# Optimization experiments

Measured on AMD Instinct MI355X. Metric: run time of the kernel, lower is better.

The kernel has to match this reference:

```python
import jax, jax.numpy as jnp
import numpy as np

N0, N1, N2, B = 1500000, 200000, 20000, 4096


def sage_conv(x_src, x_dst, src, dst, Wl, Wr, b, n_dst):
    # mean-aggregate neighbor features onto targets, then two linears + bias
    msg = x_src[src]                                             # [E, d]
    agg = jax.ops.segment_sum(msg, dst, num_segments=n_dst)       # [n_dst, d]
    cnt = jax.ops.segment_sum(jnp.ones(src.shape[0], x_src.dtype), dst, num_segments=n_dst)
    mean = agg / jnp.maximum(cnt, 1.0)[:, None]
    return mean @ Wl + x_dst @ Wr + b


def setup_inputs() -> dict:
    key = jax.random.key(0)
    ks = jax.random.split(key, 16)
    d_in, d_h, d_out = 100, 256, 47
    s = lambda k, sh, fan: jax.random.normal(k, sh, jnp.float32) * (1.0 / np.sqrt(fan))
    return {
        "x": jax.random.normal(ks[0], (N0, d_in), jnp.float32),
        "src0": jax.random.randint(ks[1], (2000000,), 0, N0),
        "dst0": jax.random.randint(ks[2], (2000000,), 0, N1),
        "src1": jax.random.randint(ks[3], (200000,), 0, N1),
        "dst1": jax.random.randint(ks[4], (200000,), 0, N2),
        "src2": jax.random.randint(ks[5], (20480,), 0, N2),
        "dst2": jax.random.randint(ks[6], (20480,), 0, B),
        "Wl0": s(ks[7], (d_in, d_h), d_in),
        "Wr0": s(ks[8], (d_in, d_h), d_in),
        "b0": jnp.zeros((d_h,), jnp.float32),
        "Wl1": s(ks[9], (d_h, d_h), d_h),
        "Wr1": s(ks[10], (d_h, d_h), d_h),
        "b1": jnp.zeros((d_h,), jnp.float32),
        "Wl2": s(ks[11], (d_h, d_out), d_h),
        "Wr2": s(ks[12], (d_h, d_out), d_h),
        "b2": jnp.zeros((d_out,), jnp.float32),
    }


def reference(x, src0, dst0, src1, dst1, src2, dst2,
              Wl0, Wr0, b0, Wl1, Wr1, b1, Wl2, Wr2, b2):
    # layer 0: sources = all sampled nodes, targets = first N1 nodes
    h = sage_conv(x, x[:N1], src0, dst0, Wl0, Wr0, b0, N1)
    h = jax.nn.relu(h)  # dropout is identity in eval mode
    # layer 1
    h = sage_conv(h, h[:N2], src1, dst1, Wl1, Wr1, b1, N2)
    h = jax.nn.relu(h)
    # layer 2 (final)
    h = sage_conv(h, h[:B], src2, dst2, Wl2, Wr2, b2, B)
    return jax.nn.log_softmax(h, axis=-1)
```

## Files before the change

### kernel.cpp

```cpp
#include <hip/hip_runtime.h>
#include <hip/hip_bf16.h>

#define N0   1500000
#define N1   200000
#define N2   20000
#define NB   4096
#define D_IN 100
#define D_H  256
#define D_OUT 47

#define K0P  224
#define K12P 512

#define SCAN_BLOCKS 256

typedef __bf16 bf16x8 __attribute__((ext_vector_type(8)));
typedef __bf16 bf16x4 __attribute__((ext_vector_type(4)));
typedef float  f32x4  __attribute__((ext_vector_type(4)));

__global__ void hist_kernel(const int* __restrict__ dst, int* __restrict__ deg, int E)
{
    int i = blockIdx.x * blockDim.x + threadIdx.x;
    if (i < E) atomicAdd(&deg[dst[i]], 1);
}

__global__ __launch_bounds__(256)
void scan_partial(const int* __restrict__ deg, int* __restrict__ partials, int n)
{
    const int b = blockIdx.x;
    const int chunk = (n + gridDim.x - 1) / gridDim.x;
    const int begin = b * chunk;
    const int end = min(begin + chunk, n);

    int s = 0;
    for (int i = begin + threadIdx.x; i < end; i += blockDim.x) s += deg[i];

    #pragma unroll
    for (int o = 32; o > 0; o >>= 1) s += __shfl_down(s, o);
    __shared__ int wsum[4];
    if ((threadIdx.x & 63) == 0) wsum[threadIdx.x >> 6] = s;
    __syncthreads();
    if (threadIdx.x == 0)
        partials[b] = wsum[0] + wsum[1] + wsum[2] + wsum[3];
}

__global__ __launch_bounds__(256)
void scan_offsets(int* __restrict__ partials, int* __restrict__ rowstart, int n)
{
    __shared__ int sm[256];
    const int t = threadIdx.x;
    sm[t] = partials[t];
    __syncthreads();
    for (int d = 1; d < 256; d <<= 1) {
        int val = sm[t];
        int oth = (t >= d) ? sm[t - d] : 0;
        __syncthreads();
        sm[t] = val + oth;
        __syncthreads();
    }
    partials[t] = (t > 0) ? sm[t - 1] : 0;
    if (t == 0) rowstart[n] = sm[255];
}

__global__ __launch_bounds__(256)
void scan_apply(const int* __restrict__ deg, const int* __restrict__ offsets,
                int* __restrict__ rowstart, int n)
{
    const int b = blockIdx.x;
    const int chunk = (n + gridDim.x - 1) / gridDim.x;
    const int begin = b * chunk;
    const int end = min(begin + chunk, n);

    __shared__ int sm[256];
    const int sub = (chunk + blockDim.x - 1) / blockDim.x;
    const int tb = begin + threadIdx.x * sub;
    const int te = min(tb + sub, end);

    int s = 0;
    for (int i = tb; i < te; ++i) s += deg[i];
    sm[threadIdx.x] = s;
    __syncthreads();
    for (int d = 1; d < 256; d <<= 1) {
        int val = sm[threadIdx.x];
        int oth = (threadIdx.x >= d) ? sm[threadIdx.x - d] : 0;
        __syncthreads();
        sm[threadIdx.x] = val + oth;
        __syncthreads();
    }
    int run = offsets[b] + ((threadIdx.x > 0) ? sm[threadIdx.x - 1] : 0);
    for (int i = tb; i < te; ++i) { rowstart[i] = run; run += deg[i]; }
}

__global__ void scatter_kernel(const int* __restrict__ src,
                               const int* __restrict__ dst,
                               const int* __restrict__ rowstart,
                               int* __restrict__ cursor,
                               int* __restrict__ csr_src, int E)
{
    int i = blockIdx.x * blockDim.x + threadIdx.x;
    if (i < E) {
        int t = dst[i];
        int pos = rowstart[t] + atomicAdd(&cursor[t], 1);
        csr_src[pos] = src[i];
    }
}

__global__ __launch_bounds__(256)
void gather_pack_l0(const float* __restrict__ x,
                    const int* __restrict__ rowstart,
                    const int* __restrict__ csr_src,
                    __bf16* __restrict__ A0, int nrows)
{
    const int wid  = (blockIdx.x * blockDim.x + threadIdx.x) >> 6;
    const int lane = threadIdx.x & 63;
    if (wid >= nrows) return;

    const int beg = rowstart[wid];
    const int end = rowstart[wid + 1];
    const bool act = lane < D_IN / 2;
    const int f = lane * 2;

    float ax[8], ay[8];
    #pragma unroll
    for (int u = 0; u < 8; ++u) { ax[u] = 0.0f; ay[u] = 0.0f; }

    int e = beg;
    for (; e + 8 <= end; e += 8) {
        int idx[8];
        #pragma unroll
        for (int u = 0; u < 8; ++u) idx[u] = csr_src[e + u];
        if (act) {
            float2 p[8];
            #pragma unroll
            for (int u = 0; u < 8; ++u)
                p[u] = *reinterpret_cast<const float2*>(x + (long)idx[u] * D_IN + f);
            #pragma unroll
            for (int u = 0; u < 8; ++u) { ax[u] += p[u].x; ay[u] += p[u].y; }
        }
    }
    for (; e + 4 <= end; e += 4) {
        int idx[4];
        #pragma unroll
        for (int u = 0; u < 4; ++u) idx[u] = csr_src[e + u];
        if (act) {
            float2 p[4];
            #pragma unroll
            for (int u = 0; u < 4; ++u)
                p[u] = *reinterpret_cast<const float2*>(x + (long)idx[u] * D_IN + f);
            #pragma unroll
            for (int u = 0; u < 4; ++u) { ax[u] += p[u].x; ay[u] += p[u].y; }
        }
    }
    for (; e < end; ++e) {
        int i0 = csr_src[e];
        if (act) {
            float2 p = *reinterpret_cast<const float2*>(x + (long)i0 * D_IN + f);
            ax[0] += p.x; ay[0] += p.y;
        }
    }

    const float inv = 1.0f / fmaxf((float)(end - beg), 1.0f);
    __bf16* o = A0 + (long)wid * K0P;
    const float* xd = x + (long)wid * D_IN;

    if (act) {
        float sx = ((ax[0] + ax[1]) + (ax[2] + ax[3])) + ((ax[4] + ax[5]) + (ax[6] + ax[7]));
        float sy = ((ay[0] + ay[1]) + (ay[2] + ay[3])) + ((ay[4] + ay[5]) + (ay[6] + ay[7]));
        o[f]     = (__bf16)(sx * inv);
        o[f + 1] = (__bf16)(sy * inv);
        float2 d = *reinterpret_cast<const float2*>(xd + f);
        o[D_IN + f]     = (__bf16)d.x;
        o[D_IN + f + 1] = (__bf16)d.y;
    }
    if (lane < K0P - 2 * D_IN) o[2 * D_IN + lane] = (__bf16)0.0f;
}

__global__ __launch_bounds__(256)
void gather_pack_h(const __bf16* __restrict__ h,
                   const int* __restrict__ rowstart,
                   const int* __restrict__ csr_src,
                   __bf16* __restrict__ Ap, int nrows)
{
    const int wid  = (blockIdx.x * blockDim.x + threadIdx.x) >> 6;
    const int lane = threadIdx.x & 63;
    if (wid >= nrows) return;

    const int beg = rowstart[wid];
    const int end = rowstart[wid + 1];
    const __bf16* hf = h + lane * 4;

    float acc[8][4];
    #pragma unroll
    for (int u = 0; u < 8; ++u)
        #pragma unroll
        for (int k = 0; k < 4; ++k) acc[u][k] = 0.0f;

    int e = beg;
    for (; e + 8 <= end; e += 8) {
        int idx[8];
        #pragma unroll
        for (int u = 0; u < 8; ++u) idx[u] = csr_src[e + u];
        bf16x4 v[8];
        #pragma unroll
        for (int u = 0; u < 8; ++u)
            v[u] = *reinterpret_cast<const bf16x4*>(hf + (long)idx[u] * D_H);
        #pragma unroll
        for (int u = 0; u < 8; ++u)
            #pragma unroll
            for (int k = 0; k < 4; ++k) acc[u][k] += (float)v[u][k];
    }
    for (; e + 4 <= end; e += 4) {
        int idx[4];
        #pragma unroll
        for (int u = 0; u < 4; ++u) idx[u] = csr_src[e + u];
        bf16x4 v[4];
        #pragma unroll
        for (int u = 0; u < 4; ++u)
            v[u] = *reinterpret_cast<const bf16x4*>(hf + (long)idx[u] * D_H);
        #pragma unroll
        for (int u = 0; u < 4; ++u)
            #pragma unroll
            for (int k = 0; k < 4; ++k) acc[u][k] += (float)v[u][k];
    }
    for (; e < end; ++e) {
        bf16x4 v = *reinterpret_cast<const bf16x4*>(hf + (long)csr_src[e] * D_H);
        #pragma unroll
        for (int k = 0; k < 4; ++k) acc[0][k] += (float)v[k];
    }

    const float inv = 1.0f / fmaxf((float)(end - beg), 1.0f);
    bf16x4 m;
    #pragma unroll
    for (int k = 0; k < 4; ++k) {
        float s = ((acc[0][k] + acc[1][k]) + (acc[2][k] + acc[3][k]))
                + ((acc[4][k] + acc[5][k]) + (acc[6][k] + acc[7][k]));
        m[k] = (__bf16)(s * inv);
    }
    *reinterpret_cast<bf16x4*>(Ap + (long)wid * K12P + lane * 4) = m;

    bf16x4 own = *reinterpret_cast<const bf16x4*>(h + (long)wid * D_H + lane * 4);
    *reinterpret_cast<bf16x4*>(Ap + (long)wid * K12P + D_H + lane * 4) = own;
}

__global__ void pack_weights_all(const float* __restrict__ Wl0, const float* __restrict__ Wr0, __bf16* __restrict__ Wp0,
                                 const float* __restrict__ Wl1, const float* __restrict__ Wr1, __bf16* __restrict__ Wp1,
                                 const float* __restrict__ Wl2, const float* __restrict__ Wr2, __bf16* __restrict__ Wp2)
{
    int b = blockIdx.x;
    const float* Wl; const float* Wr; __bf16* Wp;
    int K1, N, Kpad, n;
    if (b < 256)      { Wl = Wl0; Wr = Wr0; Wp = Wp0; K1 = D_IN; N = D_H;   Kpad = K0P;  n = b; }
    else if (b < 512) { Wl = Wl1; Wr = Wr1; Wp = Wp1; K1 = D_H;  N = D_H;   Kpad = K12P; n = b - 256; }
    else              { Wl = Wl2; Wr = Wr2; Wp = Wp2; K1 = D_H;  N = D_OUT; Kpad = K12P; n = b - 512; }

    for (int k = threadIdx.x; k < Kpad; k += blockDim.x) {
        float v = 0.0f;
        if (n < N) {
            if (k < K1)            v = Wl[(long)k * N + n];
            else if (k < 2 * K1)   v = Wr[(long)(k - K1) * N + n];
        }
        Wp[(long)n * Kpad + k] = (__bf16)v;
    }
}

#define BM 128
#define BK 32

template <int BN_T, int NT>
__global__ __launch_bounds__(NT)
void mfma_gemm(const __bf16* __restrict__ A,
               const __bf16* __restrict__ Bt,
               const float* __restrict__ bias,
               __bf16* __restrict__ Cbf,
               float* __restrict__ Cf,
               int M, int K, int Nreal, int relu)
{
    constexpr int WC = (NT / 64) / 2;
    static_assert(WC * 64 == BN_T, "wave grid must cover BN_T");
    constexpr int SIT = (BM + BN_T) * 4 / NT;
    static_assert((BM * 4) % 64 == 0, "A/B staging boundary must be wave-aligned");

    __shared__ __bf16 S[(BM + BN_T) * BK];

    const int tid  = threadIdx.x;
    const int lane = tid & 63;
    const int wv   = tid >> 6;
    const int wr   = wv / WC;
    const int wc   = wv % WC;
    const long row0 = (long)blockIdx.x * BM;
    const int  col0 = blockIdx.y * BN_T;

    f32x4 acc[4][4] = {};

    for (int k0 = 0; k0 < K; k0 += BK) {
        __syncthreads();
        #pragma unroll
        for (int i = 0; i < SIT; ++i) {
            int c  = tid + i * NT;
            int r  = c >> 2;
            int ko = (c & 3) * 8;
            const __bf16* g;
            if (r < BM) {
                long gr = row0 + r;
                if (gr > M - 1) gr = M - 1;
                g = &A[gr * K + k0 + ko];
            } else {
                g = &Bt[(long)(col0 + (r - BM)) * K + k0 + ko];
            }
            __bf16* ldsb = &S[(size_t)(i * NT + wv * 64) * 8];
            __builtin_amdgcn_global_load_lds(
                (const __attribute__((address_space(1))) void*)g,
                (__attribute__((address_space(3))) void*)ldsb,
                16, 0, 0);
        }
        __syncthreads();

        bf16x8 a[4], b[4];
        #pragma unroll
        for (int mi = 0; mi < 4; ++mi)
            a[mi] = *reinterpret_cast<const bf16x8*>(
                &S[(wr * 64 + mi * 16 + (lane & 15)) * BK + (lane >> 4) * 8]);
        #pragma unroll
        for (int ni = 0; ni < 4; ++ni)
            b[ni] = *reinterpret_cast<const bf16x8*>(
                &S[(BM + wc * 64 + ni * 16 + (lane & 15)) * BK + (lane >> 4) * 8]);

        #pragma unroll
        for (int mi = 0; mi < 4; ++mi)
            #pragma unroll
            for (int ni = 0; ni < 4; ++ni)
                acc[mi][ni] = __builtin_amdgcn_mfma_f32_16x16x32_bf16(
                    a[mi], b[ni], acc[mi][ni], 0, 0, 0);
    }

    const int colBase = col0 + wc * 64;
    #pragma unroll
    for (int mi = 0; mi < 4; ++mi) {
        const long rowBase = row0 + wr * 64 + mi * 16 + (lane >> 4) * 4;
        #pragma unroll
        for (int j = 0; j < 4; ++j) {
            long r = rowBase + j;
            if (r >= M) continue;
            #pragma unroll
            for (int ni = 0; ni < 4; ++ni) {
                int cc = colBase + ni * 16 + (lane & 15);
                if (cc >= Nreal) continue;
                float v = acc[mi][ni][j] + bias[cc];
                if (relu) v = fmaxf(v, 0.0f);
                if (Cbf) Cbf[r * Nreal + cc] = (__bf16)v;
                else     Cf [r * Nreal + cc] = v;
            }
        }
    }
}

__global__ void log_softmax_kernel(const float* __restrict__ in,
                                   float* __restrict__ out,
                                   int rows, int cols)
{
    int wave = (blockIdx.x * blockDim.x + threadIdx.x) / 64;
    int lane = threadIdx.x % 64;
    if (wave >= rows) return;

    const float* r = in + (long)wave * cols;
    float v = (lane < cols) ? r[lane] : -INFINITY;

    float m = v;
    #pragma unroll
    for (int o = 32; o > 0; o >>= 1) m = fmaxf(m, __shfl_xor(m, o));

    float e = (lane < cols) ? __expf(v - m) : 0.0f;
    float s = e;
    #pragma unroll
    for (int o = 32; o > 0; o >>= 1) s += __shfl_xor(s, o);

    float ls = logf(s);
    if (lane < cols)
        out[(long)wave * cols + lane] = v - m - ls;
}

extern "C" void kernel_launch(void* const* d_in, const int* in_sizes, int n_in,
                              void* d_out, int out_size, void* d_ws, size_t ws_size,
                              hipStream_t stream)
{
    const float* x    = (const float*)d_in[0];
    const int*   src0 = (const int*)d_in[1];
    const int*   dst0 = (const int*)d_in[2];
    const int*   src1 = (const int*)d_in[3];
    const int*   dst1 = (const int*)d_in[4];
    const int*   src2 = (const int*)d_in[5];
    const int*   dst2 = (const int*)d_in[6];
    const float* Wl0  = (const float*)d_in[7];
    const float* Wr0  = (const float*)d_in[8];
    const float* b0   = (const float*)d_in[9];
    const float* Wl1  = (const float*)d_in[10];
    const float* Wr1  = (const float*)d_in[11];
    const float* b1   = (const float*)d_in[12];
    const float* Wl2  = (const float*)d_in[13];
    const float* Wr2  = (const float*)d_in[14];
    const float* b2   = (const float*)d_in[15];
    float* out = (float*)d_out;

    const int E0 = in_sizes[1];
    const int E1 = in_sizes[3];
    const int E2 = in_sizes[5];

    char* wp = (char*)d_ws;
    auto alloc = [&](size_t bytes) -> char* {
        char* p = wp; wp += (bytes + 255) & ~(size_t)255; return p;
    };
    __bf16* A0   = (__bf16*)alloc((size_t)N1 * K0P * 2);
    __bf16* h0   = (__bf16*)alloc((size_t)N1 * D_H * 2);
    __bf16* A1   = (__bf16*)alloc((size_t)N2 * K12P * 2);
    __bf16* h1   = (__bf16*)alloc((size_t)N2 * D_H * 2);
    __bf16* A2   = (__bf16*)alloc((size_t)NB * K12P * 2);
    float*  logits = (float*)alloc((size_t)NB * D_OUT * 4);
    __bf16* Wp0  = (__bf16*)alloc((size_t)256 * K0P * 2);
    __bf16* Wp1  = (__bf16*)alloc((size_t)256 * K12P * 2);
    __bf16* Wp2  = (__bf16*)alloc((size_t)128 * K12P * 2);
    int* deg      = (int*)alloc((size_t)N1 * 4);
    int* cursor   = (int*)alloc((size_t)N1 * 4);
    int* rowstart = (int*)alloc((size_t)(N1 + 1) * 4);
    int* partials = (int*)alloc((size_t)SCAN_BLOCKS * 4);
    int* csr_src  = (int*)alloc((size_t)E0 * 4);

    pack_weights_all<<<640, 256, 0, stream>>>(Wl0, Wr0, Wp0, Wl1, Wr1, Wp1, Wl2, Wr2, Wp2);

    hipMemsetAsync(deg, 0, (size_t)N1 * 4, stream);
    hipMemsetAsync(cursor, 0, (size_t)N1 * 4, stream);
    hist_kernel<<<(E0 + 255) / 256, 256, 0, stream>>>(dst0, deg, E0);
    scan_partial<<<SCAN_BLOCKS, 256, 0, stream>>>(deg, partials, N1);
    scan_offsets<<<1, 256, 0, stream>>>(partials, rowstart, N1);
    scan_apply<<<SCAN_BLOCKS, 256, 0, stream>>>(deg, partials, rowstart, N1);
    scatter_kernel<<<(E0 + 255) / 256, 256, 0, stream>>>(src0, dst0, rowstart, cursor, csr_src, E0);
    gather_pack_l0<<<(N1 + 3) / 4, 256, 0, stream>>>(x, rowstart, csr_src, A0, N1);
    {
        dim3 grid((N1 + BM - 1) / BM, 1);
        mfma_gemm<256, 512><<<grid, 512, 0, stream>>>(A0, Wp0, b0, h0, nullptr,
                                                      N1, K0P, D_H, 1);
    }

    hipMemsetAsync(deg, 0, (size_t)N2 * 4, stream);
    hipMemsetAsync(cursor, 0, (size_t)N2 * 4, stream);
    hist_kernel<<<(E1 + 255) / 256, 256, 0, stream>>>(dst1, deg, E1);
    scan_partial<<<SCAN_BLOCKS, 256, 0, stream>>>(deg, partials, N2);
    scan_offsets<<<1, 256, 0, stream>>>(partials, rowstart, N2);
    scan_apply<<<SCAN_BLOCKS, 256, 0, stream>>>(deg, partials, rowstart, N2);
    scatter_kernel<<<(E1 + 255) / 256, 256, 0, stream>>>(src1, dst1, rowstart, cursor, csr_src, E1);
    gather_pack_h<<<(N2 + 3) / 4, 256, 0, stream>>>(h0, rowstart, csr_src, A1, N2);
    {
        dim3 grid((N2 + BM - 1) / BM, 2);
        mfma_gemm<128, 256><<<grid, 256, 0, stream>>>(A1, Wp1, b1, h1, nullptr,
                                                      N2, K12P, D_H, 1);
    }

    hipMemsetAsync(deg, 0, (size_t)NB * 4, stream);
    hipMemsetAsync(cursor, 0, (size_t)NB * 4, stream);
    hist_kernel<<<(E2 + 255) / 256, 256, 0, stream>>>(dst2, deg, E2);
    scan_partial<<<SCAN_BLOCKS, 256, 0, stream>>>(deg, partials, NB);
    scan_offsets<<<1, 256, 0, stream>>>(partials, rowstart, NB);
    scan_apply<<<SCAN_BLOCKS, 256, 0, stream>>>(deg, partials, rowstart, NB);
    scatter_kernel<<<(E2 + 255) / 256, 256, 0, stream>>>(src2, dst2, rowstart, cursor, csr_src, E2);
    gather_pack_h<<<(NB + 3) / 4, 256, 0, stream>>>(h1, rowstart, csr_src, A2, NB);
    {
        dim3 grid((NB + BM - 1) / BM, 1);
        mfma_gemm<128, 256><<<grid, 256, 0, stream>>>(A2, Wp2, b2, nullptr, logits,
                                                      NB, K12P, D_OUT, 0);
    }

    {
        int waves_per_block = 256 / 64;
        int blocks = (NB + waves_per_block - 1) / waves_per_block;
        log_softmax_kernel<<<blocks, 256, 0, stream>>>(logits, out, NB, D_OUT);
    }
}
```

Before: 634.2 us.

## Build all three layers' CSR in one pass and gather four rows per wave

The three per-layer CSR builds (memsets, histogram, three-kernel scan, scatter) are merged into one pass over a concatenated node space, so layers 1 and 2 simply index rowstart at an offset. This removes about 18 small kernel launches and memsets. The layer-0 gather now has each wave handle four destination rows at once, interleaving their neighbour loads to keep more memory requests in flight. In exchange there is more divergence when row degrees differ, and the fp32 summation order changes.

```diff
diff --git a/kernel.cpp b/kernel.cpp
--- a/kernel.cpp
+++ b/kernel.cpp
@@ -12,16 +12,25 @@
 #define K0P  224
 #define K12P 512
 
+#define NTOT (N1 + N2 + NB)
 #define SCAN_BLOCKS 256
 
 typedef __bf16 bf16x8 __attribute__((ext_vector_type(8)));
 typedef __bf16 bf16x4 __attribute__((ext_vector_type(4)));
 typedef float  f32x4  __attribute__((ext_vector_type(4)));
 
-__global__ void hist_kernel(const int* __restrict__ dst, int* __restrict__ deg, int E)
+__global__ void hist_all(const int* __restrict__ dst0, int E0,
+                         const int* __restrict__ dst1, int E1,
+                         const int* __restrict__ dst2, int E2,
+                         int* __restrict__ deg)
 {
     int i = blockIdx.x * blockDim.x + threadIdx.x;
-    if (i < E) atomicAdd(&deg[dst[i]], 1);
+    int t;
+    if (i < E0)            t = dst0[i];
+    else if (i < E0 + E1)  t = N1 + dst1[i - E0];
+    else if (i < E0 + E1 + E2) t = N1 + N2 + dst2[i - E0 - E1];
+    else return;
+    atomicAdd(&deg[t], 1);
 }
 
 __global__ __launch_bounds__(256)
@@ -91,88 +100,95 @@
     for (int i = tb; i < te; ++i) { rowstart[i] = run; run += deg[i]; }
 }
 
-__global__ void scatter_kernel(const int* __restrict__ src,
-                               const int* __restrict__ dst,
-                               const int* __restrict__ rowstart,
-                               int* __restrict__ cursor,
-                               int* __restrict__ csr_src, int E)
+__global__ void scatter_all(const int* __restrict__ src0, const int* __restrict__ dst0, int E0,
+                            const int* __restrict__ src1, const int* __restrict__ dst1, int E1,
+                            const int* __restrict__ src2, const int* __restrict__ dst2, int E2,
+                            const int* __restrict__ rowstart,
+                            int* __restrict__ cursor,
+                            int* __restrict__ csr_src)
 {
     int i = blockIdx.x * blockDim.x + threadIdx.x;
-    if (i < E) {
-        int t = dst[i];
-        int pos = rowstart[t] + atomicAdd(&cursor[t], 1);
-        csr_src[pos] = src[i];
-    }
+    int t, s;
+    if (i < E0)                { t = dst0[i];                 s = src0[i]; }
+    else if (i < E0 + E1)      { t = N1 + dst1[i - E0];       s = src1[i - E0]; }
+    else if (i < E0 + E1 + E2) { t = N1 + N2 + dst2[i - E0 - E1]; s = src2[i - E0 - E1]; }
+    else return;
+    int pos = rowstart[t] + atomicAdd(&cursor[t], 1);
+    csr_src[pos] = s;
 }
 
 __global__ __launch_bounds__(256)
 void gather_pack_l0(const float* __restrict__ x,
                     const int* __restrict__ rowstart,
-                    const int* __restrict__ csr_src,
+                    const int* __restrict__ csr,
                     __bf16* __restrict__ A0, int nrows)
 {
     const int wid  = (blockIdx.x * blockDim.x + threadIdx.x) >> 6;
     const int lane = threadIdx.x & 63;
-    if (wid >= nrows) return;
-
-    const int beg = rowstart[wid];
-    const int end = rowstart[wid + 1];
+    const int r0 = wid * 4;
+    if (r0 >= nrows) return;
+
     const bool act = lane < D_IN / 2;
     const int f = lane * 2;
-
-    float ax[8], ay[8];
-    #pragma unroll
-    for (int u = 0; u < 8; ++u) { ax[u] = 0.0f; ay[u] = 0.0f; }
-
-    int e = beg;
-    for (; e + 8 <= end; e += 8) {
-        int idx[8];
-        #pragma unroll
-        for (int u = 0; u < 8; ++u) idx[u] = csr_src[e + u];
+    const float* xf = x + f;
+
+    int cur[4], end_[4];
+    #pragma unroll
+    for (int i = 0; i < 4; ++i) {
+        int r = r0 + i;
+        cur[i]  = (r < nrows) ? rowstart[r] : 0;
+        end_[i] = (r < nrows) ? rowstart[r + 1] : 0;
+    }
+    int deg[4];
+    #pragma unroll
+    for (int i = 0; i < 4; ++i) deg[i] = end_[i] - cur[i];
+
+    float accx[4], accy[4];
+    #pragma unroll
+    for (int i = 0; i < 4; ++i) { accx[i] = 0.0f; accy[i] = 0.0f; }
+
+    while ((cur[0] < end_[0]) | (cur[1] < end_[1]) |
+           (cur[2] < end_[2]) | (cur[3] < end_[3])) {
+        float2 v[4][4];
+        #pragma unroll
+        for (int i = 0; i < 4; ++i)
+            #pragma unroll
+            for (int s = 0; s < 4; ++s) { v[i][s].x = 0.0f; v[i][s].y = 0.0f; }
+
+        #pragma unroll
+        for (int i = 0; i < 4; ++i) {
+            #pragma unroll
+            for (int s = 0; s < 4; ++s) {
+                if (cur[i] + s < end_[i]) {
+                    int idx = csr[cur[i] + s];
+                    if (act)
+                        v[i][s] = *reinterpret_cast<const float2*>(xf + (long)idx * D_IN);
+                }
+            }
+        }
+        #pragma unroll
+        for (int i = 0; i < 4; ++i) {
+            accx[i] += (v[i][0].x + v[i][1].x) + (v[i][2].x + v[i][3].x);
+            accy[i] += (v[i][0].y + v[i][1].y) + (v[i][2].y + v[i][3].y);
+            cur[i] = min(cur[i] + 4, end_[i]);
+        }
+    }
+
+    #pragma unroll
+    for (int i = 0; i < 4; ++i) {
+        int r = r0 + i;
+        if (r >= nrows) break;
+        const float inv = 1.0f / fmaxf((float)deg[i], 1.0f);
+        __bf16* o = A0 + (long)r * K0P;
         if (act) {
-            float2 p[8];
-            #pragma unroll
-            for (int u = 0; u < 8; ++u)
-                p[u] = *reinterpret_cast<const float2*>(x + (long)idx[u] * D_IN + f);
-            #pragma unroll
-            for (int u = 0; u < 8; ++u) { ax[u] += p[u].x; ay[u] += p[u].y; }
-        }
-    }
-    for (; e + 4 <= end; e += 4) {
-        int idx[4];
-        #pragma unroll
-        for (int u = 0; u < 4; ++u) idx[u] = csr_src[e + u];
-        if (act) {
-            float2 p[4];
-            #pragma unroll
-            for (int u = 0; u < 4; ++u)
-                p[u] = *reinterpret_cast<const float2*>(x + (long)idx[u] * D_IN + f);
-            #pragma unroll
-            for (int u = 0; u < 4; ++u) { ax[u] += p[u].x; ay[u] += p[u].y; }
-        }
-    }
-    for (; e < end; ++e) {
-        int i0 = csr_src[e];
-        if (act) {
-            float2 p = *reinterpret_cast<const float2*>(x + (long)i0 * D_IN + f);
-            ax[0] += p.x; ay[0] += p.y;
-        }
-    }
-
-    const float inv = 1.0f / fmaxf((float)(end - beg), 1.0f);
-    __bf16* o = A0 + (long)wid * K0P;
-    const float* xd = x + (long)wid * D_IN;
-
-    if (act) {
-        float sx = ((ax[0] + ax[1]) + (ax[2] + ax[3])) + ((ax[4] + ax[5]) + (ax[6] + ax[7]));
-        float sy = ((ay[0] + ay[1]) + (ay[2] + ay[3])) + ((ay[4] + ay[5]) + (ay[6] + ay[7]));
-        o[f]     = (__bf16)(sx * inv);
-        o[f + 1] = (__bf16)(sy * inv);
-        float2 d = *reinterpret_cast<const float2*>(xd + f);
-        o[D_IN + f]     = (__bf16)d.x;
-        o[D_IN + f + 1] = (__bf16)d.y;
-    }
-    if (lane < K0P - 2 * D_IN) o[2 * D_IN + lane] = (__bf16)0.0f;
+            o[f]     = (__bf16)(accx[i] * inv);
+            o[f + 1] = (__bf16)(accy[i] * inv);
+            float2 d = *reinterpret_cast<const float2*>(x + (long)r * D_IN + f);
+            o[D_IN + f]     = (__bf16)d.x;
+            o[D_IN + f + 1] = (__bf16)d.y;
+        }
+        if (lane < K0P - 2 * D_IN) o[2 * D_IN + lane] = (__bf16)0.0f;
+    }
 }
 
 __global__ __launch_bounds__(256)
@@ -404,6 +420,7 @@
     const int E0 = in_sizes[1];
     const int E1 = in_sizes[3];
     const int E2 = in_sizes[5];
+    const int ETOT = E0 + E1 + E2;
 
     char* wp = (char*)d_ws;
     auto alloc = [&](size_t bytes) -> char* {
@@ -418,51 +435,40 @@
     __bf16* Wp0  = (__bf16*)alloc((size_t)256 * K0P * 2);
     __bf16* Wp1  = (__bf16*)alloc((size_t)256 * K12P * 2);
     __bf16* Wp2  = (__bf16*)alloc((size_t)128 * K12P * 2);
-    int* deg      = (int*)alloc((size_t)N1 * 4);
-    int* cursor   = (int*)alloc((size_t)N1 * 4);
-    int* rowstart = (int*)alloc((size_t)(N1 + 1) * 4);
+    int* deg      = (int*)alloc((size_t)NTOT * 4);
+    int* cursor   = (int*)alloc((size_t)NTOT * 4);
+    int* rowstart = (int*)alloc((size_t)(NTOT + 1) * 4);
     int* partials = (int*)alloc((size_t)SCAN_BLOCKS * 4);
-    int* csr_src  = (int*)alloc((size_t)E0 * 4);
+    int* csr_src  = (int*)alloc((size_t)ETOT * 4);
 
     pack_weights_all<<<640, 256, 0, stream>>>(Wl0, Wr0, Wp0, Wl1, Wr1, Wp1, Wl2, Wr2, Wp2);
-
-    hipMemsetAsync(deg, 0, (size_t)N1 * 4, stream);
-    hipMemsetAsync(cursor, 0, (size_t)N1 * 4, stream);
-    hist_kernel<<<(E0 + 255) / 256, 256, 0, stream>>>(dst0, deg, E0);
-    scan_partial<<<SCAN_BLOCKS, 256, 0, stream>>>(deg, partials, N1);
-    scan_offsets<<<1, 256, 0, stream>>>(partials, rowstart, N1);
-    scan_apply<<<SCAN_BLOCKS, 256, 0, stream>>>(deg, partials, rowstart, N1);
-    scatter_kernel<<<(E0 + 255) / 256, 256, 0, stream>>>(src0, dst0, rowstart, cursor, csr_src, E0);
-    gather_pack_l0<<<(N1 + 3) / 4, 256, 0, stream>>>(x, rowstart, csr_src, A0, N1);
+    hipMemsetAsync(deg, 0, (size_t)NTOT * 4, stream);
+    hipMemsetAsync(cursor, 0, (size_t)NTOT * 4, stream);
+    hist_all<<<(ETOT + 255) / 256, 256, 0, stream>>>(dst0, E0, dst1, E1, dst2, E2, deg);
+    scan_partial<<<SCAN_BLOCKS, 256, 0, stream>>>(deg, partials, NTOT);
+    scan_offsets<<<1, 256, 0, stream>>>(partials, rowstart, NTOT);
+    scan_apply<<<SCAN_BLOCKS, 256, 0, stream>>>(deg, partials, rowstart, NTOT);
+    scatter_all<<<(ETOT + 255) / 256, 256, 0, stream>>>(src0, dst0, E0, src1, dst1, E1,
+                                                        src2, dst2, E2,
+                                                        rowstart, cursor, csr_src);
+
     {
+        int waves = (N1 + 3) / 4;
+        gather_pack_l0<<<(waves + 3) / 4, 256, 0, stream>>>(x, rowstart, csr_src, A0, N1);
         dim3 grid((N1 + BM - 1) / BM, 1);
         mfma_gemm<256, 512><<<grid, 512, 0, stream>>>(A0, Wp0, b0, h0, nullptr,
                                                       N1, K0P, D_H, 1);
     }
 
-    hipMemsetAsync(deg, 0, (size_t)N2 * 4, stream);
-    hipMemsetAsync(cursor, 0, (size_t)N2 * 4, stream);
-    hist_kernel<<<(E1 + 255) / 256, 256, 0, stream>>>(dst1, deg, E1);
-    scan_partial<<<SCAN_BLOCKS, 256, 0, stream>>>(deg, partials, N2);
-    scan_offsets<<<1, 256, 0, stream>>>(partials, rowstart, N2);
-    scan_apply<<<SCAN_BLOCKS, 256, 0, stream>>>(deg, partials, rowstart, N2);
-    scatter_kernel<<<(E1 + 255) / 256, 256, 0, stream>>>(src1, dst1, rowstart, cursor, csr_src, E1);
-    gather_pack_h<<<(N2 + 3) / 4, 256, 0, stream>>>(h0, rowstart, csr_src, A1, N2);
     {
+        gather_pack_h<<<(N2 + 3) / 4, 256, 0, stream>>>(h0, rowstart + N1, csr_src, A1, N2);
         dim3 grid((N2 + BM - 1) / BM, 2);
         mfma_gemm<128, 256><<<grid, 256, 0, stream>>>(A1, Wp1, b1, h1, nullptr,
                                                       N2, K12P, D_H, 1);
     }
 
-    hipMemsetAsync(deg, 0, (size_t)NB * 4, stream);
-    hipMemsetAsync(cursor, 0, (size_t)NB * 4, stream);
-    hist_kernel<<<(E2 + 255) / 256, 256, 0, stream>>>(dst2, deg, E2);
-    scan_partial<<<SCAN_BLOCKS, 256, 0, stream>>>(deg, partials, NB);
-    scan_offsets<<<1, 256, 0, stream>>>(partials, rowstart, NB);
-    scan_apply<<<SCAN_BLOCKS, 256, 0, stream>>>(deg, partials, rowstart, NB);
-    scatter_kernel<<<(E2 + 255) / 256, 256, 0, stream>>>(src2, dst2, rowstart, cursor, csr_src, E2);
-    gather_pack_h<<<(NB + 3) / 4, 256, 0, stream>>>(h1, rowstart, csr_src, A2, NB);
     {
+        gather_pack_h<<<(NB + 3) / 4, 256, 0, stream>>>(h1, rowstart + N1 + N2, csr_src, A2, NB);
         dim3 grid((NB + BM - 1) / BM, 1);
         mfma_gemm<128, 256><<<grid, 256, 0, stream>>>(A2, Wp2, b2, nullptr, logits,
                                                       NB, K12P, D_OUT, 0);
```

Result: slower. 745.9 us (+17.6%).

## Build CSR for all three layers in one combined histogram/scan/scatter pass

Applied to the files above, without the earlier changes.

Concatenates the destination index spaces of the three layers (offset by N1 and N1+N2) so one memset pair, one histogram, one three-stage scan and one scatter build the CSR for every layer at once. Each gather kernel then reads its layer's slice through an offset rowstart pointer. This removes about 16 small kernel launches and memsets, most of which did very little work for layers 1 and 2. The cost is a slightly larger scan, extra branching in the hist and scatter kernels, and a larger csr_src buffer.

```diff
diff --git a/kernel.cpp b/kernel.cpp
--- a/kernel.cpp
+++ b/kernel.cpp
@@ -12,16 +12,25 @@
 #define K0P  224
 #define K12P 512
 
+#define NTOT (N1 + N2 + NB)
 #define SCAN_BLOCKS 256
 
 typedef __bf16 bf16x8 __attribute__((ext_vector_type(8)));
 typedef __bf16 bf16x4 __attribute__((ext_vector_type(4)));
 typedef float  f32x4  __attribute__((ext_vector_type(4)));
 
-__global__ void hist_kernel(const int* __restrict__ dst, int* __restrict__ deg, int E)
+__global__ void hist_all(const int* __restrict__ dst0, int E0,
+                         const int* __restrict__ dst1, int E1,
+                         const int* __restrict__ dst2, int E2,
+                         int* __restrict__ deg)
 {
     int i = blockIdx.x * blockDim.x + threadIdx.x;
-    if (i < E) atomicAdd(&deg[dst[i]], 1);
+    int t;
+    if (i < E0)            t = dst0[i];
+    else if (i < E0 + E1)  t = N1 + dst1[i - E0];
+    else if (i < E0 + E1 + E2) t = N1 + N2 + dst2[i - E0 - E1];
+    else return;
+    atomicAdd(&deg[t], 1);
 }
 
 __global__ __launch_bounds__(256)
@@ -91,18 +100,21 @@
     for (int i = tb; i < te; ++i) { rowstart[i] = run; run += deg[i]; }
 }
 
-__global__ void scatter_kernel(const int* __restrict__ src,
-                               const int* __restrict__ dst,
-                               const int* __restrict__ rowstart,
-                               int* __restrict__ cursor,
-                               int* __restrict__ csr_src, int E)
+__global__ void scatter_all(const int* __restrict__ src0, const int* __restrict__ dst0, int E0,
+                            const int* __restrict__ src1, const int* __restrict__ dst1, int E1,
+                            const int* __restrict__ src2, const int* __restrict__ dst2, int E2,
+                            const int* __restrict__ rowstart,
+                            int* __restrict__ cursor,
+                            int* __restrict__ csr_src)
 {
     int i = blockIdx.x * blockDim.x + threadIdx.x;
-    if (i < E) {
-        int t = dst[i];
-        int pos = rowstart[t] + atomicAdd(&cursor[t], 1);
-        csr_src[pos] = src[i];
-    }
+    int t, s;
+    if (i < E0)                { t = dst0[i];                 s = src0[i]; }
+    else if (i < E0 + E1)      { t = N1 + dst1[i - E0];       s = src1[i - E0]; }
+    else if (i < E0 + E1 + E2) { t = N1 + N2 + dst2[i - E0 - E1]; s = src2[i - E0 - E1]; }
+    else return;
+    int pos = rowstart[t] + atomicAdd(&cursor[t], 1);
+    csr_src[pos] = s;
 }
 
 __global__ __launch_bounds__(256)
@@ -404,6 +416,7 @@
     const int E0 = in_sizes[1];
     const int E1 = in_sizes[3];
     const int E2 = in_sizes[5];
+    const int ETOT = E0 + E1 + E2;
 
     char* wp = (char*)d_ws;
     auto alloc = [&](size_t bytes) -> char* {
@@ -418,51 +431,39 @@
     __bf16* Wp0  = (__bf16*)alloc((size_t)256 * K0P * 2);
     __bf16* Wp1  = (__bf16*)alloc((size_t)256 * K12P * 2);
     __bf16* Wp2  = (__bf16*)alloc((size_t)128 * K12P * 2);
-    int* deg      = (int*)alloc((size_t)N1 * 4);
-    int* cursor   = (int*)alloc((size_t)N1 * 4);
-    int* rowstart = (int*)alloc((size_t)(N1 + 1) * 4);
+    int* deg      = (int*)alloc((size_t)NTOT * 4);
+    int* cursor   = (int*)alloc((size_t)NTOT * 4);
+    int* rowstart = (int*)alloc((size_t)(NTOT + 1) * 4);
     int* partials = (int*)alloc((size_t)SCAN_BLOCKS * 4);
-    int* csr_src  = (int*)alloc((size_t)E0 * 4);
+    int* csr_src  = (int*)alloc((size_t)ETOT * 4);
 
     pack_weights_all<<<640, 256, 0, stream>>>(Wl0, Wr0, Wp0, Wl1, Wr1, Wp1, Wl2, Wr2, Wp2);
-
-    hipMemsetAsync(deg, 0, (size_t)N1 * 4, stream);
-    hipMemsetAsync(cursor, 0, (size_t)N1 * 4, stream);
-    hist_kernel<<<(E0 + 255) / 256, 256, 0, stream>>>(dst0, deg, E0);
-    scan_partial<<<SCAN_BLOCKS, 256, 0, stream>>>(deg, partials, N1);
-    scan_offsets<<<1, 256, 0, stream>>>(partials, rowstart, N1);
-    scan_apply<<<SCAN_BLOCKS, 256, 0, stream>>>(deg, partials, rowstart, N1);
-    scatter_kernel<<<(E0 + 255) / 256, 256, 0, stream>>>(src0, dst0, rowstart, cursor, csr_src, E0);
-    gather_pack_l0<<<(N1 + 3) / 4, 256, 0, stream>>>(x, rowstart, csr_src, A0, N1);
+    hipMemsetAsync(deg, 0, (size_t)NTOT * 4, stream);
+    hipMemsetAsync(cursor, 0, (size_t)NTOT * 4, stream);
+    hist_all<<<(ETOT + 255) / 256, 256, 0, stream>>>(dst0, E0, dst1, E1, dst2, E2, deg);
+    scan_partial<<<SCAN_BLOCKS, 256, 0, stream>>>(deg, partials, NTOT);
+    scan_offsets<<<1, 256, 0, stream>>>(partials, rowstart, NTOT);
+    scan_apply<<<SCAN_BLOCKS, 256, 0, stream>>>(deg, partials, rowstart, NTOT);
+    scatter_all<<<(ETOT + 255) / 256, 256, 0, stream>>>(src0, dst0, E0, src1, dst1, E1,
+                                                        src2, dst2, E2,
+                                                        rowstart, cursor, csr_src);
+
     {
+        gather_pack_l0<<<(N1 + 3) / 4, 256, 0, stream>>>(x, rowstart, csr_src, A0, N1);
         dim3 grid((N1 + BM - 1) / BM, 1);
         mfma_gemm<256, 512><<<grid, 512, 0, stream>>>(A0, Wp0, b0, h0, nullptr,
                                                       N1, K0P, D_H, 1);
     }
 
-    hipMemsetAsync(deg, 0, (size_t)N2 * 4, stream);
-    hipMemsetAsync(cursor, 0, (size_t)N2 * 4, stream);
-    hist_kernel<<<(E1 + 255) / 256, 256, 0, stream>>>(dst1, deg, E1);
-    scan_partial<<<SCAN_BLOCKS, 256, 0, stream>>>(deg, partials, N2);
-    scan_offsets<<<1, 256, 0, stream>>>(partials, rowstart, N2);
-    scan_apply<<<SCAN_BLOCKS, 256, 0, stream>>>(deg, partials, rowstart, N2);
-    scatter_kernel<<<(E1 + 255) / 256, 256, 0, stream>>>(src1, dst1, rowstart, cursor, csr_src, E1);
-    gather_pack_h<<<(N2 + 3) / 4, 256, 0, stream>>>(h0, rowstart, csr_src, A1, N2);
     {
+        gather_pack_h<<<(N2 + 3) / 4, 256, 0, stream>>>(h0, rowstart + N1, csr_src, A1, N2);
         dim3 grid((N2 + BM - 1) / BM, 2);
         mfma_gemm<128, 256><<<grid, 256, 0, stream>>>(A1, Wp1, b1, h1, nullptr,
                                                       N2, K12P, D_H, 1);
     }
 
-    hipMemsetAsync(deg, 0, (size_t)NB * 4, stream);
-    hipMemsetAsync(cursor, 0, (size_t)NB * 4, stream);
-    hist_kernel<<<(E2 + 255) / 256, 256, 0, stream>>>(dst2, deg, E2);
-    scan_partial<<<SCAN_BLOCKS, 256, 0, stream>>>(deg, partials, NB);
-    scan_offsets<<<1, 256, 0, stream>>>(partials, rowstart, NB);
-    scan_apply<<<SCAN_BLOCKS, 256, 0, stream>>>(deg, partials, rowstart, NB);
-    scatter_kernel<<<(E2 + 255) / 256, 256, 0, stream>>>(src2, dst2, rowstart, cursor, csr_src, E2);
-    gather_pack_h<<<(NB + 3) / 4, 256, 0, stream>>>(h1, rowstart, csr_src, A2, NB);
     {
+        gather_pack_h<<<(NB + 3) / 4, 256, 0, stream>>>(h1, rowstart + N1 + N2, csr_src, A2, NB);
         dim3 grid((NB + BM - 1) / BM, 1);
         mfma_gemm<128, 256><<<grid, 256, 0, stream>>>(A2, Wp2, b2, nullptr, logits,
                                                       NB, K12P, D_OUT, 0);
```

New measurement: 599.7 us. -5.4%, faster.
